# Optimization experiments

Measured on AMD Instinct MI355X. Metric: run time of the kernel, lower is better.

Reference implementation:

```python
import jax, jax.numpy as jnp
import numpy as np
from jax import lax

BITW = 1
BITA = 3


def _ste_round(x, n):
    # round with straight-through gradient (Round -> Identity override)
    return x + lax.stop_gradient(jnp.round(x * n) / n - x)


def _quantize_active(x, bitA):
    # cabs: clip |x| to [0, 1], then k-bit uniform quantization with STE round
    x = jnp.minimum(1.0, jnp.abs(x))
    if bitA == 32:
        return x
    n = float(2 ** bitA - 1)
    return _ste_round(x, n)


def _quantize_weight(w, bitW):
    if bitW == 32:
        return w
    if bitW == 1:
        # sign with STE (Sign -> Identity): grad w.r.t. w is 1
        E = lax.stop_gradient(jnp.mean(jnp.abs(w)))
        y = w / E
        return (y + lax.stop_gradient(jnp.sign(y) - y)) * E
    n = float(2 ** bitW - 1)
    w = jnp.clip(w * 0.5 + 0.5, 0.0, 1.0)
    return 2.0 * _ste_round(w, n) - 1.0


def setup_inputs() -> dict:
    key = jax.random.key(0)
    kx, kw, kb = jax.random.split(key, 3)
    x = jax.random.normal(kx, (32, 56, 56, 256), dtype=jnp.float32)
    W = jax.random.normal(kw, (3, 3, 256, 256), dtype=jnp.float32) * 0.02  # HWIO
    b = jax.random.normal(kb, (256,), dtype=jnp.float32) * 0.01
    return {"x": x, "W": W, "b": b}


def reference(x, W, b):
    xq = _quantize_active(x, BITA)          # [N,H,W,C] quantized activations
    wq = _quantize_weight(W, BITW)          # [kh,kw,Cin,Cout] binarized weights
    out = lax.conv_general_dilated(
        xq, wq,
        window_strides=(1, 1),
        padding="SAME",
        dimension_numbers=("NHWC", "HWIO", "NHWC"),
    )
    return out + b  # act = identity
```

## Files before the change

### kernel.cpp

```cpp
#include <hip/hip_runtime.h>

typedef __attribute__((ext_vector_type(4))) int int4v;
typedef __attribute__((ext_vector_type(16))) int int16v;

#define NPIX 100352
#define PPIX 107648
#define KTAP 2304
#define LDK 144
#define BSZ (256 * LDK)
#define CHB (PPIX * 16)

__global__ __launch_bounds__(256) void quant_w_kernel(const float* __restrict__ Wm,
                                                      signed char* __restrict__ Bt,
                                                      float* __restrict__ Esum) {
  __shared__ signed char sT[64][80];
  __shared__ float red[4];
  const int k0 = blockIdx.x * 64;
  const int c0 = blockIdx.y * 64;
  const int t = threadIdx.x;
  const int cc = t & 63;
  const int r0 = (t >> 6) * 16;
  float s = 0.f;
#pragma unroll
  for (int i = 0; i < 16; ++i) {
    const int k = r0 + i;
    float w = Wm[(long)(k0 + k) * 256 + c0 + cc];
    s += fabsf(w);
    sT[cc][k] = (signed char)((w > 0.f) ? 1 : ((w < 0.f) ? -1 : 0));
  }
#pragma unroll
  for (int o = 32; o > 0; o >>= 1) s += __shfl_down(s, o, 64);
  if ((t & 63) == 0) red[t >> 6] = s;
  __syncthreads();
  if (t == 0) atomicAdd(Esum, red[0] + red[1] + red[2] + red[3]);
  const int co = t >> 2;
  const int kc = (t & 3) * 16;
  int4v v = *(const int4v*)&sT[co][kc];
  *(int4v*)(Bt + (long)(c0 + co) * KTAP + k0 + kc) = v;
}

__global__ __launch_bounds__(256) void quant_x_kernel(const float* __restrict__ x,
                                                      signed char* __restrict__ xqT) {
  const int pix = blockIdx.x * 256 + threadIdx.x;
  if (pix >= PPIX) return;
  const int c = blockIdx.y;
  const int q1 = pix / 58;
  const int wp = pix - q1 * 58;
  const int n  = q1 / 58;
  const int hp = q1 - n * 58;
  int4v out = {0, 0, 0, 0};
  if ((unsigned)(hp - 1) < 56u && (unsigned)(wp - 1) < 56u) {
    const int src = n * 3136 + (hp - 1) * 56 + (wp - 1);
    const float4* px = (const float4*)(x + (long)src * 256 + c * 16);
#pragma unroll
    for (int j = 0; j < 4; ++j) {
      float4 v = px[j];
      unsigned q;
      q  = (unsigned)(int)rintf(fminf(1.f, fabsf(v.x)) * 7.f);
      q |= ((unsigned)(int)rintf(fminf(1.f, fabsf(v.y)) * 7.f)) << 8;
      q |= ((unsigned)(int)rintf(fminf(1.f, fabsf(v.z)) * 7.f)) << 16;
      q |= ((unsigned)(int)rintf(fminf(1.f, fabsf(v.w)) * 7.f)) << 24;
      out[j] = (int)q;
    }
  }
  *(int4v*)(xqT + (long)c * CHB + pix * 16) = out;
}


__global__ __launch_bounds__(256, 2) void conv_kernel(const signed char* __restrict__ xqT,
                                                      const signed char* __restrict__ Bt,
                                                      const float* __restrict__ bias,
                                                      const float* __restrict__ Esum,
                                                      float* __restrict__ out) {
  __shared__ signed char Bs[2 * BSZ];

  const int t = threadIdx.x;
  const int lane = t & 63;
  const int wid = t >> 6;
  const int bid = blockIdx.x;
  const int tile = (bid & 7) * 98 + (bid >> 3);
  const int m0 = tile * 128;
  const int wm = (wid & 1) * 64;
  const int wn = (wid >> 1) * 128;
  const int lrow = lane & 31;
  const int half = lane >> 5;

  int pp0, pp1;
  {
    const int p0 = m0 + wm + lrow;
    const int n0 = p0 / 3136, r0 = p0 - n0 * 3136;
    const int h0 = r0 / 56, w0 = r0 - h0 * 56;
    pp0 = (n0 * 58 + h0 + 1) * 58 + (w0 + 1);
    const int p1 = p0 + 32;
    const int n1 = p1 / 3136, r1 = p1 - n1 * 3136;
    const int h1 = r1 / 56, w1 = r1 - h1 * 56;
    pp1 = (n1 * 58 + h1 + 1) * 58 + (w1 + 1);
  }

  auto aptr = [&](int u, int pp) -> const signed char* {
    const int tp = u >> 1;
    const int dp = (tp / 3 - 1) * 58 + (tp % 3) - 1;
    return xqT + (((u & 1) * 8 + half) * PPIX + pp + dp) * 16;
  };
  const int ks_step = 2 * CHB;

  const int brow = t >> 3;
  const int bcol = (t & 7) * 16;
  const int gb = brow * KTAP + bcol;
  const int lb = brow * LDK + bcol;

  int16v acc[2][4];
#pragma unroll
  for (int a = 0; a < 2; ++a)
#pragma unroll
    for (int b = 0; b < 4; ++b)
#pragma unroll
      for (int r = 0; r < 16; ++r) acc[a][b][r] = 0;

  int4v raA0 = *(const int4v*)aptr(0, pp0);
  int4v raA1 = *(const int4v*)aptr(0, pp1);
  int4v rb[8];
#pragma unroll
  for (int i = 0; i < 8; ++i) rb[i] = *(const int4v*)(Bt + gb + i * (32 * KTAP));
#pragma unroll
  for (int i = 0; i < 8; ++i) *(int4v*)(Bs + lb + i * (32 * LDK)) = rb[i];
#pragma unroll
  for (int i = 0; i < 8; ++i) rb[i] = *(const int4v*)(Bt + gb + 128 + i * (32 * KTAP));
  asm volatile("s_waitcnt lgkmcnt(0)" ::: "memory");
  __builtin_amdgcn_s_barrier();
  __builtin_amdgcn_sched_barrier(0);

  for (int s = 0; s < 18; ++s) {
    signed char* Bcur = Bs + (s & 1) * BSZ;
    signed char* Bnxt = Bs + ((~s) & 1) * BSZ;
    const signed char* a0p = aptr(s, pp0);
    const signed char* a1p = aptr(s, pp1);
    const signed char* n0p = aptr(s < 17 ? s + 1 : 17, pp0);
    const signed char* n1p = aptr(s < 17 ? s + 1 : 17, pp1);

    if (s + 1 < 18) {
#pragma unroll
      for (int i = 0; i < 8; ++i) *(int4v*)(Bnxt + lb + i * (32 * LDK)) = rb[i];
    }
    if (s + 2 < 18) {
      const int ko2 = (s + 2) * 128;
#pragma unroll
      for (int i = 0; i < 8; ++i) rb[i] = *(const int4v*)(Bt + gb + ko2 + i * (32 * KTAP));
    }

#pragma unroll
    for (int ks = 0; ks < 4; ++ks) {
      int4v nx0 = *(const int4v*)((ks < 3) ? (a0p + (ks + 1) * ks_step) : n0p);
      int4v nx1 = *(const int4v*)((ks < 3) ? (a1p + (ks + 1) * ks_step) : n1p);
      const int ko = ks * 32 + half * 16;
      int4v b0 = *(const int4v*)(Bcur + (wn + lrow) * LDK + ko);
      int4v b1 = *(const int4v*)(Bcur + (wn + 32 + lrow) * LDK + ko);
      int4v b2 = *(const int4v*)(Bcur + (wn + 64 + lrow) * LDK + ko);
      int4v b3 = *(const int4v*)(Bcur + (wn + 96 + lrow) * LDK + ko);
      __builtin_amdgcn_s_setprio(1);
      acc[0][0] = __builtin_amdgcn_mfma_i32_32x32x32_i8(raA0, b0, acc[0][0], 0, 0, 0);
      acc[0][1] = __builtin_amdgcn_mfma_i32_32x32x32_i8(raA0, b1, acc[0][1], 0, 0, 0);
      acc[0][2] = __builtin_amdgcn_mfma_i32_32x32x32_i8(raA0, b2, acc[0][2], 0, 0, 0);
      acc[0][3] = __builtin_amdgcn_mfma_i32_32x32x32_i8(raA0, b3, acc[0][3], 0, 0, 0);
      acc[1][0] = __builtin_amdgcn_mfma_i32_32x32x32_i8(raA1, b0, acc[1][0], 0, 0, 0);
      acc[1][1] = __builtin_amdgcn_mfma_i32_32x32x32_i8(raA1, b1, acc[1][1], 0, 0, 0);
      acc[1][2] = __builtin_amdgcn_mfma_i32_32x32x32_i8(raA1, b2, acc[1][2], 0, 0, 0);
      acc[1][3] = __builtin_amdgcn_mfma_i32_32x32x32_i8(raA1, b3, acc[1][3], 0, 0, 0);
      __builtin_amdgcn_s_setprio(0);
      raA0 = nx0; raA1 = nx1;
    }

    if (s < 17) {
      asm volatile("s_waitcnt lgkmcnt(0)" ::: "memory");
      __builtin_amdgcn_sched_barrier(0);
      __builtin_amdgcn_s_barrier();
      __builtin_amdgcn_sched_barrier(0);
    }
  }

  const float scale = Esum[0] * (1.0f / (589824.0f * 7.0f));
#pragma unroll
  for (int mt = 0; mt < 2; ++mt)
#pragma unroll
    for (int nt = 0; nt < 4; ++nt) {
      const int col = wn + nt * 32 + lrow;
      const float bv = bias[col];
#pragma unroll
      for (int r = 0; r < 16; ++r) {
        const int row = (r & 3) + 8 * (r >> 2) + 4 * (lane >> 5);
        const int m = m0 + wm + mt * 32 + row;
        out[(long)m * 256 + col] = (float)acc[mt][nt][r] * scale + bv;
      }
    }
}

extern "C" void kernel_launch(void* const* d_in, const int* in_sizes, int n_in,
                              void* d_out, int out_size, void* d_ws, size_t ws_size,
                              hipStream_t stream) {
  const float* x    = (const float*)d_in[0];
  const float* Wm   = (const float*)d_in[1];
  const float* bias = (const float*)d_in[2];
  float* out = (float*)d_out;

  float* Esum = (float*)d_ws;
  signed char* Bt = (signed char*)d_ws + 256;
  signed char* xqT = (signed char*)d_ws + 256 + 589824;

  hipMemsetAsync(d_ws, 0, 4, stream);
  quant_w_kernel<<<dim3(36, 4), 256, 0, stream>>>(Wm, Bt, Esum);
  quant_x_kernel<<<dim3(421, 16), 256, 0, stream>>>(x, xqT);
  conv_kernel<<<784, 256, 0, stream>>>(xqT, Bt, bias, Esum, out);
}
```

Measured before the change: 265.3 us.

## Split conv output channels into two tiles, single-buffer B, coalesce activation quantization

The conv kernel now tiles each block as 128 pixels by 128 output channels instead of 128 by 256, which doubles the grid. B is held in a single LDS tile covering one full tap (256 K values) per stage, with 9 stages instead of 18, and occupancy is raised to 3 blocks. This cuts LDS and register use, but every A fragment is now loaded twice across the two channel halves. The activation quantizer now reads x fully coalesced as float4 and scatters 4-byte writes into the padded layout. A separate memset zeroes the halo, which adds a large fill pass.

```diff
diff --git a/kernel.cpp b/kernel.cpp
--- a/kernel.cpp
+++ b/kernel.cpp
@@ -6,9 +6,9 @@
 #define NPIX 100352
 #define PPIX 107648
 #define KTAP 2304
-#define LDK 144
-#define BSZ (256 * LDK)
 #define CHB (PPIX * 16)
+#define LDB 272
+#define BTILE (128 * LDB)
 
 __global__ __launch_bounds__(256) void quant_w_kernel(const float* __restrict__ Wm,
                                                       signed char* __restrict__ Bt,
@@ -41,140 +41,110 @@
 
 __global__ __launch_bounds__(256) void quant_x_kernel(const float* __restrict__ x,
                                                       signed char* __restrict__ xqT) {
-  const int pix = blockIdx.x * 256 + threadIdx.x;
-  if (pix >= PPIX) return;
-  const int c = blockIdx.y;
-  const int q1 = pix / 58;
-  const int wp = pix - q1 * 58;
-  const int n  = q1 / 58;
-  const int hp = q1 - n * 58;
-  int4v out = {0, 0, 0, 0};
-  if ((unsigned)(hp - 1) < 56u && (unsigned)(wp - 1) < 56u) {
-    const int src = n * 3136 + (hp - 1) * 56 + (wp - 1);
-    const float4* px = (const float4*)(x + (long)src * 256 + c * 16);
-#pragma unroll
-    for (int j = 0; j < 4; ++j) {
-      float4 v = px[j];
-      unsigned q;
-      q  = (unsigned)(int)rintf(fminf(1.f, fabsf(v.x)) * 7.f);
-      q |= ((unsigned)(int)rintf(fminf(1.f, fabsf(v.y)) * 7.f)) << 8;
-      q |= ((unsigned)(int)rintf(fminf(1.f, fabsf(v.z)) * 7.f)) << 16;
-      q |= ((unsigned)(int)rintf(fminf(1.f, fabsf(v.w)) * 7.f)) << 24;
-      out[j] = (int)q;
-    }
-  }
-  *(int4v*)(xqT + (long)c * CHB + pix * 16) = out;
+  const int tid = blockIdx.x * 256 + threadIdx.x;
+  float4 v = ((const float4*)x)[tid];
+  unsigned q;
+  q  = (unsigned)(int)rintf(fminf(1.f, fabsf(v.x)) * 7.f);
+  q |= ((unsigned)(int)rintf(fminf(1.f, fabsf(v.y)) * 7.f)) << 8;
+  q |= ((unsigned)(int)rintf(fminf(1.f, fabsf(v.z)) * 7.f)) << 16;
+  q |= ((unsigned)(int)rintf(fminf(1.f, fabsf(v.w)) * 7.f)) << 24;
+  const int pix = tid >> 6;
+  const int l = tid & 63;
+  const int n = pix / 3136;
+  const int rem = pix - n * 3136;
+  const int h = rem / 56, w = rem - (rem / 56) * 56;
+  const int pp = (n * 58 + h + 1) * 58 + (w + 1);
+  const int c = l >> 2, j = l & 3;
+  *(unsigned*)(xqT + (long)c * CHB + pp * 16 + j * 4) = q;
 }
 
-
-__global__ __launch_bounds__(256, 2) void conv_kernel(const signed char* __restrict__ xqT,
+__global__ __launch_bounds__(256, 3) void conv_kernel(const signed char* __restrict__ xqT,
                                                       const signed char* __restrict__ Bt,
                                                       const float* __restrict__ bias,
                                                       const float* __restrict__ Esum,
                                                       float* __restrict__ out) {
-  __shared__ signed char Bs[2 * BSZ];
+  __shared__ signed char Bs[BTILE];
 
   const int t = threadIdx.x;
   const int lane = t & 63;
   const int wid = t >> 6;
   const int bid = blockIdx.x;
-  const int tile = (bid & 7) * 98 + (bid >> 3);
-  const int m0 = tile * 128;
+  const int tile = (bid & 7) * 196 + (bid >> 3);
+  const int m0 = (tile >> 1) * 128;
+  const int n0 = (tile & 1) * 128;
   const int wm = (wid & 1) * 64;
-  const int wn = (wid >> 1) * 128;
+  const int wn = (wid >> 1) * 64;
   const int lrow = lane & 31;
   const int half = lane >> 5;
 
-  int pp0, pp1;
+  const signed char *ap0, *ap1;
   {
     const int p0 = m0 + wm + lrow;
-    const int n0 = p0 / 3136, r0 = p0 - n0 * 3136;
-    const int h0 = r0 / 56, w0 = r0 - h0 * 56;
-    pp0 = (n0 * 58 + h0 + 1) * 58 + (w0 + 1);
+    const int n_ = p0 / 3136, r_ = p0 - n_ * 3136;
+    const int h_ = r_ / 56, w_ = r_ - h_ * 56;
+    ap0 = xqT + (long)half * CHB + ((n_ * 58 + h_ + 1) * 58 + (w_ + 1)) * 16;
     const int p1 = p0 + 32;
-    const int n1 = p1 / 3136, r1 = p1 - n1 * 3136;
-    const int h1 = r1 / 56, w1 = r1 - h1 * 56;
-    pp1 = (n1 * 58 + h1 + 1) * 58 + (w1 + 1);
+    const int n2 = p1 / 3136, r2 = p1 - n2 * 3136;
+    const int h2 = r2 / 56, w2 = r2 - h2 * 56;
+    ap1 = xqT + (long)half * CHB + ((n2 * 58 + h2 + 1) * 58 + (w2 + 1)) * 16;
   }
+  auto dp16 = [](int tap) { return ((tap / 3 - 1) * 58 + (tap % 3) - 1) * 16; };
 
-  auto aptr = [&](int u, int pp) -> const signed char* {
-    const int tp = u >> 1;
-    const int dp = (tp / 3 - 1) * 58 + (tp % 3) - 1;
-    return xqT + (((u & 1) * 8 + half) * PPIX + pp + dp) * 16;
-  };
-  const int ks_step = 2 * CHB;
+  const int brow = t >> 4;
+  const int bcol = (t & 15) * 16;
+  const int gb0 = (n0 + brow) * KTAP + bcol;
+  const int lb0 = brow * LDB + bcol;
 
-  const int brow = t >> 3;
-  const int bcol = (t & 7) * 16;
-  const int gb = brow * KTAP + bcol;
-  const int lb = brow * LDK + bcol;
-
-  int16v acc[2][4];
+  int16v acc[2][2];
 #pragma unroll
   for (int a = 0; a < 2; ++a)
 #pragma unroll
-    for (int b = 0; b < 4; ++b)
+    for (int b = 0; b < 2; ++b)
 #pragma unroll
       for (int r = 0; r < 16; ++r) acc[a][b][r] = 0;
 
-  int4v raA0 = *(const int4v*)aptr(0, pp0);
-  int4v raA1 = *(const int4v*)aptr(0, pp1);
   int4v rb[8];
 #pragma unroll
-  for (int i = 0; i < 8; ++i) rb[i] = *(const int4v*)(Bt + gb + i * (32 * KTAP));
+  for (int i = 0; i < 8; ++i) rb[i] = *(const int4v*)(Bt + gb0 + i * (16 * KTAP));
+  int4v raA0 = *(const int4v*)(ap0 + dp16(0));
+  int4v raA1 = *(const int4v*)(ap1 + dp16(0));
+
+  for (int s = 0; s < 9; ++s) {
+    if (s) __builtin_amdgcn_s_barrier();
 #pragma unroll
-  for (int i = 0; i < 8; ++i) *(int4v*)(Bs + lb + i * (32 * LDK)) = rb[i];
+    for (int i = 0; i < 8; ++i) *(int4v*)(Bs + lb0 + i * (16 * LDB)) = rb[i];
+    asm volatile("s_waitcnt lgkmcnt(0)" ::: "memory");
+    __builtin_amdgcn_sched_barrier(0);
+    __builtin_amdgcn_s_barrier();
+    __builtin_amdgcn_sched_barrier(0);
+
+    if (s + 1 < 9) {
+      const int go = (s + 1) * 256;
 #pragma unroll
-  for (int i = 0; i < 8; ++i) rb[i] = *(const int4v*)(Bt + gb + 128 + i * (32 * KTAP));
-  asm volatile("s_waitcnt lgkmcnt(0)" ::: "memory");
-  __builtin_amdgcn_s_barrier();
-  __builtin_amdgcn_sched_barrier(0);
-
-  for (int s = 0; s < 18; ++s) {
-    signed char* Bcur = Bs + (s & 1) * BSZ;
-    signed char* Bnxt = Bs + ((~s) & 1) * BSZ;
-    const signed char* a0p = aptr(s, pp0);
-    const signed char* a1p = aptr(s, pp1);
-    const signed char* n0p = aptr(s < 17 ? s + 1 : 17, pp0);
-    const signed char* n1p = aptr(s < 17 ? s + 1 : 17, pp1);
-
-    if (s + 1 < 18) {
-#pragma unroll
-      for (int i = 0; i < 8; ++i) *(int4v*)(Bnxt + lb + i * (32 * LDK)) = rb[i];
-    }
-    if (s + 2 < 18) {
-      const int ko2 = (s + 2) * 128;
-#pragma unroll
-      for (int i = 0; i < 8; ++i) rb[i] = *(const int4v*)(Bt + gb + ko2 + i * (32 * KTAP));
+      for (int i = 0; i < 8; ++i)
+        rb[i] = *(const int4v*)(Bt + gb0 + go + i * (16 * KTAP));
     }
 
+    const signed char* a0s = ap0 + dp16(s);
+    const signed char* a1s = ap1 + dp16(s);
+    const int dnx = dp16(s + 1 < 9 ? s + 1 : s);
+
 #pragma unroll
-    for (int ks = 0; ks < 4; ++ks) {
-      int4v nx0 = *(const int4v*)((ks < 3) ? (a0p + (ks + 1) * ks_step) : n0p);
-      int4v nx1 = *(const int4v*)((ks < 3) ? (a1p + (ks + 1) * ks_step) : n1p);
+    for (int ks = 0; ks < 8; ++ks) {
+      int4v nx0 = *(const int4v*)((ks < 7) ? (a0s + (ks + 1) * (2 * CHB))
+                                           : (ap0 + dnx));
+      int4v nx1 = *(const int4v*)((ks < 7) ? (a1s + (ks + 1) * (2 * CHB))
+                                           : (ap1 + dnx));
       const int ko = ks * 32 + half * 16;
-      int4v b0 = *(const int4v*)(Bcur + (wn + lrow) * LDK + ko);
-      int4v b1 = *(const int4v*)(Bcur + (wn + 32 + lrow) * LDK + ko);
-      int4v b2 = *(const int4v*)(Bcur + (wn + 64 + lrow) * LDK + ko);
-      int4v b3 = *(const int4v*)(Bcur + (wn + 96 + lrow) * LDK + ko);
+      int4v b0 = *(const int4v*)(Bs + (wn + lrow) * LDB + ko);
+      int4v b1 = *(const int4v*)(Bs + (wn + 32 + lrow) * LDB + ko);
       __builtin_amdgcn_s_setprio(1);
       acc[0][0] = __builtin_amdgcn_mfma_i32_32x32x32_i8(raA0, b0, acc[0][0], 0, 0, 0);
       acc[0][1] = __builtin_amdgcn_mfma_i32_32x32x32_i8(raA0, b1, acc[0][1], 0, 0, 0);
-      acc[0][2] = __builtin_amdgcn_mfma_i32_32x32x32_i8(raA0, b2, acc[0][2], 0, 0, 0);
-      acc[0][3] = __builtin_amdgcn_mfma_i32_32x32x32_i8(raA0, b3, acc[0][3], 0, 0, 0);
       acc[1][0] = __builtin_amdgcn_mfma_i32_32x32x32_i8(raA1, b0, acc[1][0], 0, 0, 0);
       acc[1][1] = __builtin_amdgcn_mfma_i32_32x32x32_i8(raA1, b1, acc[1][1], 0, 0, 0);
-      acc[1][2] = __builtin_amdgcn_mfma_i32_32x32x32_i8(raA1, b2, acc[1][2], 0, 0, 0);
-      acc[1][3] = __builtin_amdgcn_mfma_i32_32x32x32_i8(raA1, b3, acc[1][3], 0, 0, 0);
       __builtin_amdgcn_s_setprio(0);
       raA0 = nx0; raA1 = nx1;
-    }
-
-    if (s < 17) {
-      asm volatile("s_waitcnt lgkmcnt(0)" ::: "memory");
-      __builtin_amdgcn_sched_barrier(0);
-      __builtin_amdgcn_s_barrier();
-      __builtin_amdgcn_sched_barrier(0);
     }
   }
 
@@ -182,12 +152,12 @@
 #pragma unroll
   for (int mt = 0; mt < 2; ++mt)
 #pragma unroll
-    for (int nt = 0; nt < 4; ++nt) {
-      const int col = wn + nt * 32 + lrow;
+    for (int nt = 0; nt < 2; ++nt) {
+      const int col = n0 + wn + nt * 32 + lrow;
       const float bv = bias[col];
 #pragma unroll
       for (int r = 0; r < 16; ++r) {
-        const int row = (r & 3) + 8 * (r >> 2) + 4 * (lane >> 5);
+        const int row = (r & 3) + 8 * (r >> 2) + 4 * half;
         const int m = m0 + wm + mt * 32 + row;
         out[(long)m * 256 + col] = (float)acc[mt][nt][r] * scale + bv;
       }
@@ -203,11 +173,12 @@
   float* out = (float*)d_out;
 
   float* Esum = (float*)d_ws;
-  signed char* Bt = (signed char*)d_ws + 256;
+  signed char* Bt  = (signed char*)d_ws + 256;
   signed char* xqT = (signed char*)d_ws + 256 + 589824;
 
   hipMemsetAsync(d_ws, 0, 4, stream);
+  hipMemsetAsync(xqT, 0, 27557888, stream);
   quant_w_kernel<<<dim3(36, 4), 256, 0, stream>>>(Wm, Bt, Esum);
-  quant_x_kernel<<<dim3(421, 16), 256, 0, stream>>>(x, xqT);
-  conv_kernel<<<784, 256, 0, stream>>>(xqT, Bt, bias, Esum, out);
+  quant_x_kernel<<<25088, 256, 0, stream>>>(x, xqT);
+  conv_kernel<<<1568, 256, 0, stream>>>(xqT, Bt, bias, Esum, out);
 }
```

After: 252.0 us. 1.05x faster.
